# Performance work log

Measured on AMD Instinct MI355X. Metric: run time of the kernel, lower is better.

The kernel has to match this reference:

```python
import jax, jax.numpy as jnp
import numpy as np

U, I, T, D, A = 100000, 50000, 512, 64, 64
B, RU, RI = 2048, 50, 50


def _xavier(key, shape):
    fan_in, fan_out = shape[0], shape[1]
    lim = jnp.sqrt(6.0 / (fan_in + fan_out)).astype(jnp.float32)
    return jax.random.uniform(key, shape, jnp.float32, -lim, lim)


def setup_inputs() -> dict:
    key = jax.random.key(0)
    ks = jax.random.split(key, 16)
    return {
        "user": jax.random.randint(ks[0], (B,), 0, U),
        "item": jax.random.randint(ks[1], (B,), 0, I),
        "user_r_topic": jax.random.uniform(ks[2], (B, RU, T), jnp.float32),
        "item_r_topic": jax.random.uniform(ks[3], (B, RI, T), jnp.float32),
        "user_embed_w": 0.05 * jax.random.normal(ks[4], (U, D), jnp.float32),
        "item_embed_w": 0.05 * jax.random.normal(ks[5], (I, D), jnp.float32),
        "user_att_w": 0.05 * jax.random.normal(ks[6], (U, D), jnp.float32),
        "item_att_w": 0.05 * jax.random.normal(ks[7], (I, D), jnp.float32),
        "topic_embed_w": 0.05 * jax.random.normal(ks[8], (T, D), jnp.float32),
        "fc_u_w": _xavier(ks[9], (D, A)), "fc_u_b": jnp.zeros((A,), jnp.float32),
        "fc_ru_w": _xavier(ks[10], (D, A)), "fc_ru_b": jnp.zeros((A,), jnp.float32),
        "fc_i_w": _xavier(ks[11], (D, A)), "fc_i_b": jnp.zeros((A,), jnp.float32),
        "fc_ri_w": _xavier(ks[12], (D, A)), "fc_ri_b": jnp.zeros((A,), jnp.float32),
        "h_u_w": _xavier(ks[13], (A, 1)), "h_u_b": jnp.zeros((1,), jnp.float32),
        "h_i_w": _xavier(ks[14], (A, 1)), "h_i_b": jnp.zeros((1,), jnp.float32),
        "fc_pre_w": _xavier(ks[15], (2 * D, 1)), "fc_pre_b": jnp.zeros((1,), jnp.float32),
    }


def _branch(ids, emb_w, att_w, r_topic, topic_w, fc_a_w, fc_a_b, fc_r_w, fc_r_b, h_w, h_b):
    # embedding lookups
    emb = emb_w[ids]            # [B, D]
    att = att_w[ids]            # [B, D]
    # broadcast mul + sum over topics == matmul with topic table: [B, R, D]
    review = jnp.einsum("brt,td->brd", r_topic, topic_w)
    # attention scores over reviews
    s = jax.nn.relu((att @ fc_a_w + fc_a_b)[:, None, :] + review @ fc_r_w + fc_r_b)
    w = jax.nn.softmax((s @ h_w)[..., 0] + h_b[0], axis=1)   # [B, R]
    feat = jnp.einsum("br,brd->bd", w, review)               # attention pooling
    # (feat[:,None,:] * topic_emphasize).sum(dim=1) == feat * topic_w.sum(0)
    feat = feat * jnp.sum(topic_w, axis=0)
    return emb, feat


def reference(user, item, user_r_topic, item_r_topic,
              user_embed_w, item_embed_w, user_att_w, item_att_w, topic_embed_w,
              fc_u_w, fc_u_b, fc_ru_w, fc_ru_b, fc_i_w, fc_i_b, fc_ri_w, fc_ri_b,
              h_u_w, h_u_b, h_i_w, h_i_b, fc_pre_w, fc_pre_b):
    u_emb, u_feat = _branch(user, user_embed_w, user_att_w, user_r_topic, topic_embed_w,
                            fc_u_w, fc_u_b, fc_ru_w, fc_ru_b, h_u_w, h_u_b)
    i_emb, i_feat = _branch(item, item_embed_w, item_att_w, item_r_topic, topic_embed_w,
                            fc_i_w, fc_i_b, fc_ri_w, fc_ri_b, h_i_w, h_i_b)
    tmp = jnp.concatenate([u_feat + u_emb, i_feat + i_emb], axis=1)  # [B, 2D]
    pred = jax.nn.relu(tmp @ fc_pre_w + fc_pre_b)                    # [B, 1]
    return pred[:, 0]
```

## Files before the change

kernel.cpp:

```cpp
#include <hip/hip_runtime.h>
#include <cstdint>
#include <cstddef>

#define NB 2048
#define NT 512
#define ND 64
#define NR 50
#define NE 2
#define REVP 68
#define BH 32768

typedef __attribute__((ext_vector_type(8))) short bf16x8;
typedef __attribute__((ext_vector_type(4))) float f32x4;

__device__ inline unsigned short f2bf_rne(float x) {
    unsigned int u = __float_as_uint(x);
    u += 0x7fffu + ((u >> 16) & 1u);
    return (unsigned short)(u >> 16);
}

__device__ inline bf16x8 cvt8_rne(float4 v0, float4 v1) {
    union { unsigned int u[4]; bf16x8 v; } P;
    asm("v_cvt_pk_bf16_f32 %0, %1, %2" : "=v"(P.u[0]) : "v"(v0.x), "v"(v0.y));
    asm("v_cvt_pk_bf16_f32 %0, %1, %2" : "=v"(P.u[1]) : "v"(v0.z), "v"(v0.w));
    asm("v_cvt_pk_bf16_f32 %0, %1, %2" : "=v"(P.u[2]) : "v"(v1.x), "v"(v1.y));
    asm("v_cvt_pk_bf16_f32 %0, %1, %2" : "=v"(P.u[3]) : "v"(v1.z), "v"(v1.w));
    return P.v;
}

__device__ inline void gload16(const void* gsrc, void* ldst) {
    __builtin_amdgcn_global_load_lds(
        (const __attribute__((address_space(1))) unsigned int*)gsrc,
        (__attribute__((address_space(3))) unsigned int*)ldst, 16, 0, 0);
}

__global__ __launch_bounds__(256) void prep_kernel(
    const float* __restrict__ tw,
    const float* __restrict__ fc_u_w, const float* __restrict__ fc_ru_w,
    const float* __restrict__ fc_i_w, const float* __restrict__ fc_ri_w,
    unsigned short* __restrict__ bhi,
    unsigned short* __restrict__ fuhi, unsigned short* __restrict__ fihi)
{
    int i = blockIdx.x * 256 + threadIdx.x;
    if (i < 32768) {
        int j  = i & 7;
        int l  = (i >> 3) & 63;
        int n  = (i >> 9) & 3;
        int kk = i >> 11;
        int t = kk * 32 + ((l >> 4) << 3) + j;
        int d = n * 16 + (l & 15);
        bhi[i] = f2bf_rne(tw[t * ND + d]);
    } else {
        int q = i - 32768;
        int br = q >> 13;
        int e = q & 8191;
        int j  = e & 7;
        int l  = (e >> 3) & 63;
        int n  = (e >> 9) & 3;
        int kk = e >> 11;
        int k = kk * 32 + ((l >> 4) << 3) + j;
        int col = n * 16 + (l & 15);
        const float* W = (k < 64) ? (br ? fc_ri_w : fc_ru_w)
                                  : (br ? fc_i_w  : fc_u_w);
        unsigned short hi = f2bf_rne(W[(k & 63) * ND + col]);
        if (br) fihi[e] = hi; else fuhi[e] = hi;
    }
}

__global__ __launch_bounds__(256) void colsum_kernel(const float* __restrict__ tw,
                                                     float* __restrict__ colsum) {
    __shared__ float part[4][ND];
    int d = threadIdx.x & 63, p = threadIdx.x >> 6;
    float s = 0.f;
    for (int t = p; t < NT; t += 4) s += tw[t * ND + d];
    part[p][d] = s;
    __syncthreads();
    if (threadIdx.x < ND)
        colsum[d] = part[0][d] + part[1][d] + part[2][d] + part[3][d];
}

#define AISS2(T, e, COL)                                                       \
    float4 aA_##T##_0, aA_##T##_1;                                             \
    {                                                                          \
        const float* _p = arowp[e] + (size_t)rowc * NT + (COL);                \
        asm volatile("global_load_dwordx4 %0, %1, off"                         \
                     : "=v"(aA_##T##_0) : "v"(_p) : "memory");                 \
        asm volatile("global_load_dwordx4 %0, %1, off"                         \
                     : "=v"(aA_##T##_1) : "v"(_p + 4) : "memory");             \
    }
#define AISS8(T, e, h, qh)                                                     \
    AISS2(T##_0, e, (h) * 256 + ((qh) * 4 + 0) * 32 + g * 8)                   \
    AISS2(T##_1, e, (h) * 256 + ((qh) * 4 + 1) * 32 + g * 8)                   \
    AISS2(T##_2, e, (h) * 256 + ((qh) * 4 + 2) * 32 + g * 8)                   \
    AISS2(T##_3, e, (h) * 256 + ((qh) * 4 + 3) * 32 + g * 8)

#define ARET(T, N)                                                             \
    union { unsigned int u[4]; bf16x8 v; } fr_##T;                             \
    asm volatile("s_waitcnt vmcnt(" #N ")\n\t"                                 \
                 "v_cvt_pk_bf16_f32 %0, %4, %5\n\t"                            \
                 "v_cvt_pk_bf16_f32 %1, %6, %7\n\t"                            \
                 "v_cvt_pk_bf16_f32 %2, %8, %9\n\t"                            \
                 "v_cvt_pk_bf16_f32 %3, %10, %11"                              \
                 : "=&v"(fr_##T.u[0]), "=&v"(fr_##T.u[1]),                     \
                   "=&v"(fr_##T.u[2]), "=&v"(fr_##T.u[3])                      \
                 : "v"(aA_##T##_0.x), "v"(aA_##T##_0.y),                       \
                   "v"(aA_##T##_0.z), "v"(aA_##T##_0.w),                       \
                   "v"(aA_##T##_1.x), "v"(aA_##T##_1.y),                       \
                   "v"(aA_##T##_1.z), "v"(aA_##T##_1.w)                        \
                 : "memory");
#define ARETQ(T0, T1)                                                          \
    ARET(T0##_0, 14) ARET(T0##_1, 12) ARET(T0##_2, 10) ARET(T0##_3, 8)         \
    ARET(T1##_0, 6)  ARET(T1##_1, 4)  ARET(T1##_2, 2)  ARET(T1##_3, 0)
#define QCOMP(T0, T1, qh)                                                      \
    kstep((qh) * 4 + 0, fr_##T0##_0.v, fr_##T1##_0.v);                         \
    kstep((qh) * 4 + 1, fr_##T0##_1.v, fr_##T1##_1.v);                         \
    kstep((qh) * 4 + 2, fr_##T0##_2.v, fr_##T1##_2.v);                         \
    kstep((qh) * 4 + 3, fr_##T0##_3.v, fr_##T1##_3.v);

__global__ __launch_bounds__(256, 3) void branch_kernel(
    const int* __restrict__ user, const int* __restrict__ item,
    const float* __restrict__ user_r_topic, const float* __restrict__ item_r_topic,
    const float* __restrict__ user_embed_w, const float* __restrict__ item_embed_w,
    const float* __restrict__ user_att_w, const float* __restrict__ item_att_w,
    const unsigned short* __restrict__ bhi,
    const unsigned short* __restrict__ fuhi, const unsigned short* __restrict__ fihi,
    const float* __restrict__ fc_u_b, const float* __restrict__ fc_ru_b,
    const float* __restrict__ fc_i_b, const float* __restrict__ fc_ri_b,
    const float* __restrict__ h_u_w, const float* __restrict__ h_u_b,
    const float* __restrict__ h_i_w, const float* __restrict__ h_i_b,
    const float* __restrict__ colsum,
    float* __restrict__ u_vec, float* __restrict__ i_vec)
{
    __shared__ __align__(16) unsigned char arena[BH];
    __shared__ float lds_logit[NE][NR + 2];

    const int tid = threadIdx.x, wave = tid >> 6, lane = tid & 63;
    const int g = lane >> 4, c16 = lane & 15;

    const int E0 = blockIdx.x * NE;
    const int branch = E0 >> 11;

    const int*   ids     = branch ? item           : user;
    const float* r_topic = branch ? item_r_topic   : user_r_topic;
    const float* emb_w   = branch ? item_embed_w   : user_embed_w;
    const float* att_w   = branch ? item_att_w     : user_att_w;
    const unsigned short* fhi = branch ? fihi : fuhi;
    const float* fc_a_b  = branch ? fc_i_b         : fc_u_b;
    const float* fc_r_b  = branch ? fc_ri_b        : fc_ru_b;
    const float* h_w     = branch ? h_i_w          : h_u_w;
    const float* h_b     = branch ? h_i_b          : h_u_b;
    float*       out_vec = branch ? i_vec          : u_vec;

    const int rowg = wave * 16 + c16;
    const int rowc = rowg < NR ? rowg : NR - 1;

    int bidx[NE], idv[NE];
    const float* arowp[NE];
#pragma unroll
    for (int e = 0; e < NE; ++e) {
        bidx[e] = (E0 + e) & (NB - 1);
        idv[e]  = ids[bidx[e]];
        arowp[e] = r_topic + (size_t)bidx[e] * NR * NT;
    }

    auto stageB = [&](int h) {
        const unsigned char* src = (const unsigned char*)bhi + (size_t)h * BH;
#pragma unroll
        for (int i = 0; i < 8; ++i) {
            size_t off = (size_t)(i * 256 + tid) * 16;
            gload16(src + off, arena + off);
        }
    };

    f32x4 acc[NE][4];
#pragma unroll
    for (int e = 0; e < NE; ++e)
#pragma unroll
        for (int n = 0; n < 4; ++n) acc[e][n] = (f32x4){0.f, 0.f, 0.f, 0.f};

    auto kstep = [&](int klq, bf16x8 f0, bf16x8 f1) {
#pragma unroll
        for (int n = 0; n < 4; ++n) {
            bf16x8 bh = *reinterpret_cast<const bf16x8*>(
                arena + (size_t)((klq * 4 + n) * 64 + lane) * 16);
            acc[0][n] = __builtin_amdgcn_mfma_f32_16x16x32_bf16(f0, bh, acc[0][n], 0, 0, 0);
            acc[1][n] = __builtin_amdgcn_mfma_f32_16x16x32_bf16(f1, bh, acc[1][n], 0, 0, 0);
        }
    };

    stageB(0);
    AISS8(h0q0e0, 0, 0, 0) AISS8(h0q0e1, 1, 0, 0)
    asm volatile("s_waitcnt vmcnt(16)" ::: "memory");
    __builtin_amdgcn_sched_barrier(0);
    __builtin_amdgcn_s_barrier();
    __builtin_amdgcn_sched_barrier(0);
    ARETQ(h0q0e0, h0q0e1)
    QCOMP(h0q0e0, h0q0e1, 0)
    AISS8(h0q1e0, 0, 0, 1) AISS8(h0q1e1, 1, 0, 1)
    ARETQ(h0q1e0, h0q1e1)
    QCOMP(h0q1e0, h0q1e1, 1)
    __builtin_amdgcn_sched_barrier(0);
    __builtin_amdgcn_s_barrier();
    __builtin_amdgcn_sched_barrier(0);

    stageB(1);
    AISS8(h1q0e0, 0, 1, 0) AISS8(h1q0e1, 1, 1, 0)
    asm volatile("s_waitcnt vmcnt(16)" ::: "memory");
    __builtin_amdgcn_sched_barrier(0);
    __builtin_amdgcn_s_barrier();
    __builtin_amdgcn_sched_barrier(0);
    ARETQ(h1q0e0, h1q0e1)
    QCOMP(h1q0e0, h1q0e1, 0)
    AISS8(h1q1e0, 0, 1, 1) AISS8(h1q1e1, 1, 1, 1)
    ARETQ(h1q1e0, h1q1e1)
    QCOMP(h1q1e0, h1q1e1, 1)

    __syncthreads();
    float (*rev)[NR][REVP] = reinterpret_cast<float(*)[NR][REVP]>(arena);
#pragma unroll
    for (int e = 0; e < NE; ++e)
#pragma unroll
        for (int n = 0; n < 4; ++n)
#pragma unroll
            for (int r4 = 0; r4 < 4; ++r4) {
                int r = wave * 16 + g * 4 + r4;
                if (r < NR) rev[e][r][n * 16 + c16] = acc[e][n][r4];
            }

    f32x4 s4[NE][4];
#pragma unroll
    for (int e = 0; e < NE; ++e)
#pragma unroll
        for (int n = 0; n < 4; ++n) s4[e][n] = (f32x4){0.f, 0.f, 0.f, 0.f};

#pragma unroll
    for (int kk2 = 0; kk2 < 4; ++kk2) {
        bf16x8 bh[4];
#pragma unroll
        for (int n = 0; n < 4; ++n)
            bh[n] = *(reinterpret_cast<const bf16x8*>(fhi + (size_t)(kk2 * 4 + n) * 512) + lane);
#pragma unroll
        for (int e = 0; e < NE; ++e) {
            bf16x8 ah;
            if (kk2 < 2) {
                const float* rp = &rev[e][rowc][kk2 * 32 + g * 8];
                ah = cvt8_rne(*reinterpret_cast<const float4*>(rp),
                              *reinterpret_cast<const float4*>(rp + 4));
            } else {
                const float* ap = att_w + (size_t)idv[e] * ND + (kk2 - 2) * 32 + g * 8;
                ah = cvt8_rne(*reinterpret_cast<const float4*>(ap),
                              *reinterpret_cast<const float4*>(ap + 4));
            }
#pragma unroll
            for (int n = 0; n < 4; ++n)
                s4[e][n] = __builtin_amdgcn_mfma_f32_16x16x32_bf16(ah, bh[n], s4[e][n], 0, 0, 0);
        }
    }

    const float hb = h_b[0];
#pragma unroll
    for (int e = 0; e < NE; ++e) {
        float p0 = 0.f, p1 = 0.f, p2 = 0.f, p3 = 0.f;
#pragma unroll
        for (int n = 0; n < 4; ++n) {
            float hwn = h_w[n * 16 + c16];
            float bs = fc_r_b[n * 16 + c16] + fc_a_b[n * 16 + c16];
            p0 = fmaf(fmaxf(s4[e][n][0] + bs, 0.f), hwn, p0);
            p1 = fmaf(fmaxf(s4[e][n][1] + bs, 0.f), hwn, p1);
            p2 = fmaf(fmaxf(s4[e][n][2] + bs, 0.f), hwn, p2);
            p3 = fmaf(fmaxf(s4[e][n][3] + bs, 0.f), hwn, p3);
        }
#pragma unroll
        for (int off = 1; off < 16; off <<= 1) {
            p0 += __shfl_xor(p0, off);
            p1 += __shfl_xor(p1, off);
            p2 += __shfl_xor(p2, off);
            p3 += __shfl_xor(p3, off);
        }
        if (c16 == 0) {
            int rb = wave * 16 + g * 4;
            if (rb + 0 < NR) lds_logit[e][rb + 0] = p0 + hb;
            if (rb + 1 < NR) lds_logit[e][rb + 1] = p1 + hb;
            if (rb + 2 < NR) lds_logit[e][rb + 2] = p2 + hb;
            if (rb + 3 < NR) lds_logit[e][rb + 3] = p3 + hb;
        }
    }
    __syncthreads();

    if (wave < NE) {
        const int e = wave;
        const int b = bidx[e];
        const int id = idv[e];
        float m = -1e30f;
        for (int r = 0; r < NR; ++r) m = fmaxf(m, lds_logit[e][r]);
        float sum = 0.f;
        for (int r = 0; r < NR; ++r) sum += __expf(lds_logit[e][r] - m);
        float inv = 1.f / sum;
        float feat = 0.f;
        for (int r = 0; r < NR; ++r)
            feat = fmaf(__expf(lds_logit[e][r] - m), rev[e][r][lane], feat);
        feat *= inv;
        out_vec[(size_t)b * ND + lane] = feat * colsum[lane] + emb_w[(size_t)id * ND + lane];
    }
}

__global__ __launch_bounds__(64) void final_kernel(
    const float* __restrict__ u_vec, const float* __restrict__ i_vec,
    const float* __restrict__ fc_pre_w, const float* __restrict__ fc_pre_b,
    float* __restrict__ out)
{
    int b = blockIdx.x, lane = threadIdx.x;
    float v = u_vec[(size_t)b * ND + lane] * fc_pre_w[lane]
            + i_vec[(size_t)b * ND + lane] * fc_pre_w[ND + lane];
#pragma unroll
    for (int off = 32; off; off >>= 1) v += __shfl_xor(v, off);
    if (lane == 0) out[b] = fmaxf(v + fc_pre_b[0], 0.f);
}

extern "C" void kernel_launch(void* const* d_in, const int* in_sizes, int n_in,
                              void* d_out, int out_size, void* d_ws, size_t ws_size,
                              hipStream_t stream) {
    (void)in_sizes; (void)n_in; (void)out_size; (void)ws_size;

    const int*   user         = (const int*)d_in[0];
    const int*   item         = (const int*)d_in[1];
    const float* user_r_topic = (const float*)d_in[2];
    const float* item_r_topic = (const float*)d_in[3];
    const float* user_embed_w = (const float*)d_in[4];
    const float* item_embed_w = (const float*)d_in[5];
    const float* user_att_w   = (const float*)d_in[6];
    const float* item_att_w   = (const float*)d_in[7];
    const float* topic_w      = (const float*)d_in[8];
    const float* fc_u_w       = (const float*)d_in[9];
    const float* fc_u_b       = (const float*)d_in[10];
    const float* fc_ru_w      = (const float*)d_in[11];
    const float* fc_ru_b      = (const float*)d_in[12];
    const float* fc_i_w       = (const float*)d_in[13];
    const float* fc_i_b       = (const float*)d_in[14];
    const float* fc_ri_w      = (const float*)d_in[15];
    const float* fc_ri_b      = (const float*)d_in[16];
    const float* h_u_w        = (const float*)d_in[17];
    const float* h_u_b        = (const float*)d_in[18];
    const float* h_i_w        = (const float*)d_in[19];
    const float* h_i_b        = (const float*)d_in[20];
    const float* fc_pre_w     = (const float*)d_in[21];
    const float* fc_pre_b     = (const float*)d_in[22];

    unsigned short* bhi  = (unsigned short*)d_ws;
    unsigned short* fuhi = bhi + 32768;
    unsigned short* fihi = fuhi + 8192;
    float* colsum = (float*)(fihi + 8192);
    float* u_vec  = colsum + 64;
    float* i_vec  = u_vec + NB * ND;

    prep_kernel<<<192, 256, 0, stream>>>(topic_w, fc_u_w, fc_ru_w, fc_i_w, fc_ri_w,
                                         bhi, fuhi, fihi);
    colsum_kernel<<<1, 256, 0, stream>>>(topic_w, colsum);

    branch_kernel<<<(2 * NB) / NE, 256, 0, stream>>>(
        user, item, user_r_topic, item_r_topic,
        user_embed_w, item_embed_w, user_att_w, item_att_w,
        bhi, fuhi, fihi,
        fc_u_b, fc_ru_b, fc_i_b, fc_ri_b,
        h_u_w, h_u_b, h_i_w, h_i_b,
        colsum, u_vec, i_vec);

    final_kernel<<<NB, 64, 0, stream>>>(u_vec, i_vec, fc_pre_w, fc_pre_b,
                                        (float*)d_out);
}
```

Before: 124.1 us.

## Process four entities per block with full B tile staged once in LDS

Each block now handles four batch entities instead of two and stages the entire 64KB bf16 topic-weight table into LDS in one pass, so the second half-stage and its barrier go away. A-operand loads are software-pipelined per entity: each entity's fragments are converted while the next entity's loads are in flight. This cuts the number of blocks and amortizes the B-table load over twice as many entities. In exchange, occupancy drops (launch bounds from 3 to 2 blocks per CU, larger LDS), and more loads are kept in flight, which raises register pressure.

New measurement: 127.8 us. 1.03x slower.

```diff
diff --git a/kernel.cpp b/kernel.cpp
--- a/kernel.cpp
+++ b/kernel.cpp
@@ -6,9 +6,9 @@
 #define NT 512
 #define ND 64
 #define NR 50
-#define NE 2
+#define NE 4
 #define REVP 68
-#define BH 32768
+#define BFULL 65536
 
 typedef __attribute__((ext_vector_type(8))) short bf16x8;
 typedef __attribute__((ext_vector_type(4))) float f32x4;
@@ -88,13 +88,17 @@
         asm volatile("global_load_dwordx4 %0, %1, off"                         \
                      : "=v"(aA_##T##_1) : "v"(_p + 4) : "memory");             \
     }
-#define AISS8(T, e, h, qh)                                                     \
-    AISS2(T##_0, e, (h) * 256 + ((qh) * 4 + 0) * 32 + g * 8)                   \
-    AISS2(T##_1, e, (h) * 256 + ((qh) * 4 + 1) * 32 + g * 8)                   \
-    AISS2(T##_2, e, (h) * 256 + ((qh) * 4 + 2) * 32 + g * 8)                   \
-    AISS2(T##_3, e, (h) * 256 + ((qh) * 4 + 3) * 32 + g * 8)
-
-#define ARET(T, N)                                                             \
+#define AISS16(T, e, h)                                                        \
+    AISS2(T##_0, e, (h) * 256 + 0 * 32 + g * 8)                                \
+    AISS2(T##_1, e, (h) * 256 + 1 * 32 + g * 8)                                \
+    AISS2(T##_2, e, (h) * 256 + 2 * 32 + g * 8)                                \
+    AISS2(T##_3, e, (h) * 256 + 3 * 32 + g * 8)                                \
+    AISS2(T##_4, e, (h) * 256 + 4 * 32 + g * 8)                                \
+    AISS2(T##_5, e, (h) * 256 + 5 * 32 + g * 8)                                \
+    AISS2(T##_6, e, (h) * 256 + 6 * 32 + g * 8)                                \
+    AISS2(T##_7, e, (h) * 256 + 7 * 32 + g * 8)
+
+#define FRAG(T, N)                                                             \
     union { unsigned int u[4]; bf16x8 v; } fr_##T;                             \
     asm volatile("s_waitcnt vmcnt(" #N ")\n\t"                                 \
                  "v_cvt_pk_bf16_f32 %0, %4, %5\n\t"                            \
@@ -108,16 +112,19 @@
                    "v"(aA_##T##_1.x), "v"(aA_##T##_1.y),                       \
                    "v"(aA_##T##_1.z), "v"(aA_##T##_1.w)                        \
                  : "memory");
-#define ARETQ(T0, T1)                                                          \
-    ARET(T0##_0, 14) ARET(T0##_1, 12) ARET(T0##_2, 10) ARET(T0##_3, 8)         \
-    ARET(T1##_0, 6)  ARET(T1##_1, 4)  ARET(T1##_2, 2)  ARET(T1##_3, 0)
-#define QCOMP(T0, T1, qh)                                                      \
-    kstep((qh) * 4 + 0, fr_##T0##_0.v, fr_##T1##_0.v);                         \
-    kstep((qh) * 4 + 1, fr_##T0##_1.v, fr_##T1##_1.v);                         \
-    kstep((qh) * 4 + 2, fr_##T0##_2.v, fr_##T1##_2.v);                         \
-    kstep((qh) * 4 + 3, fr_##T0##_3.v, fr_##T1##_3.v);
-
-__global__ __launch_bounds__(256, 3) void branch_kernel(
+#define ARETH(T)                                                               \
+    FRAG(T##_0, 30) FRAG(T##_1, 28) FRAG(T##_2, 26) FRAG(T##_3, 24)            \
+    FRAG(T##_4, 22) FRAG(T##_5, 20) FRAG(T##_6, 18) FRAG(T##_7, 16)
+#define ARETL(T)                                                               \
+    FRAG(T##_0, 14) FRAG(T##_1, 12) FRAG(T##_2, 10) FRAG(T##_3, 8)             \
+    FRAG(T##_4, 6)  FRAG(T##_5, 4)  FRAG(T##_6, 2)  FRAG(T##_7, 0)
+#define QCOMP8(T, e, h)                                                        \
+    kstep((h) * 8 + 0, fr_##T##_0.v, e); kstep((h) * 8 + 1, fr_##T##_1.v, e);  \
+    kstep((h) * 8 + 2, fr_##T##_2.v, e); kstep((h) * 8 + 3, fr_##T##_3.v, e);  \
+    kstep((h) * 8 + 4, fr_##T##_4.v, e); kstep((h) * 8 + 5, fr_##T##_5.v, e);  \
+    kstep((h) * 8 + 6, fr_##T##_6.v, e); kstep((h) * 8 + 7, fr_##T##_7.v, e);
+
+__global__ __launch_bounds__(256, 2) void branch_kernel(
     const int* __restrict__ user, const int* __restrict__ item,
     const float* __restrict__ user_r_topic, const float* __restrict__ item_r_topic,
     const float* __restrict__ user_embed_w, const float* __restrict__ item_embed_w,
@@ -131,7 +138,7 @@
     const float* __restrict__ colsum,
     float* __restrict__ u_vec, float* __restrict__ i_vec)
 {
-    __shared__ __align__(16) unsigned char arena[BH];
+    __shared__ __align__(16) unsigned char arena[BFULL];
     __shared__ float lds_logit[NE][NR + 2];
 
     const int tid = threadIdx.x, wave = tid >> 6, lane = tid & 63;
@@ -163,57 +170,43 @@
         arowp[e] = r_topic + (size_t)bidx[e] * NR * NT;
     }
 
-    auto stageB = [&](int h) {
-        const unsigned char* src = (const unsigned char*)bhi + (size_t)h * BH;
-#pragma unroll
-        for (int i = 0; i < 8; ++i) {
-            size_t off = (size_t)(i * 256 + tid) * 16;
-            gload16(src + off, arena + off);
-        }
-    };
-
     f32x4 acc[NE][4];
 #pragma unroll
     for (int e = 0; e < NE; ++e)
 #pragma unroll
         for (int n = 0; n < 4; ++n) acc[e][n] = (f32x4){0.f, 0.f, 0.f, 0.f};
 
-    auto kstep = [&](int klq, bf16x8 f0, bf16x8 f1) {
+    auto kstep = [&](int kk, bf16x8 f, int e) {
 #pragma unroll
         for (int n = 0; n < 4; ++n) {
             bf16x8 bh = *reinterpret_cast<const bf16x8*>(
-                arena + (size_t)((klq * 4 + n) * 64 + lane) * 16);
-            acc[0][n] = __builtin_amdgcn_mfma_f32_16x16x32_bf16(f0, bh, acc[0][n], 0, 0, 0);
-            acc[1][n] = __builtin_amdgcn_mfma_f32_16x16x32_bf16(f1, bh, acc[1][n], 0, 0, 0);
+                arena + (size_t)((kk * 4 + n) * 64 + lane) * 16);
+            acc[e][n] = __builtin_amdgcn_mfma_f32_16x16x32_bf16(f, bh, acc[e][n], 0, 0, 0);
         }
     };
 
-    stageB(0);
-    AISS8(h0q0e0, 0, 0, 0) AISS8(h0q0e1, 1, 0, 0)
-    asm volatile("s_waitcnt vmcnt(16)" ::: "memory");
+    {
+#pragma unroll
+        for (int i = 0; i < 16; ++i) {
+            size_t off = (size_t)(i * 256 + tid) * 16;
+            gload16((const unsigned char*)bhi + off, arena + off);
+        }
+    }
+    AISS16(A0, 0, 0)
+    AISS16(A1, 1, 0)
+    asm volatile("s_waitcnt vmcnt(32)" ::: "memory");
     __builtin_amdgcn_sched_barrier(0);
     __builtin_amdgcn_s_barrier();
     __builtin_amdgcn_sched_barrier(0);
-    ARETQ(h0q0e0, h0q0e1)
-    QCOMP(h0q0e0, h0q0e1, 0)
-    AISS8(h0q1e0, 0, 0, 1) AISS8(h0q1e1, 1, 0, 1)
-    ARETQ(h0q1e0, h0q1e1)
-    QCOMP(h0q1e0, h0q1e1, 1)
-    __builtin_amdgcn_sched_barrier(0);
-    __builtin_amdgcn_s_barrier();
-    __builtin_amdgcn_sched_barrier(0);
-
-    stageB(1);
-    AISS8(h1q0e0, 0, 1, 0) AISS8(h1q0e1, 1, 1, 0)
-    asm volatile("s_waitcnt vmcnt(16)" ::: "memory");
-    __builtin_amdgcn_sched_barrier(0);
-    __builtin_amdgcn_s_barrier();
-    __builtin_amdgcn_sched_barrier(0);
-    ARETQ(h1q0e0, h1q0e1)
-    QCOMP(h1q0e0, h1q0e1, 0)
-    AISS8(h1q1e0, 0, 1, 1) AISS8(h1q1e1, 1, 1, 1)
-    ARETQ(h1q1e0, h1q1e1)
-    QCOMP(h1q1e0, h1q1e1, 1)
+
+    ARETH(A0) AISS16(A2, 2, 0) QCOMP8(A0, 0, 0)
+    ARETH(A1) AISS16(A3, 3, 0) QCOMP8(A1, 1, 0)
+    ARETH(A2) AISS16(B0, 0, 1) QCOMP8(A2, 2, 0)
+    ARETH(A3) AISS16(B1, 1, 1) QCOMP8(A3, 3, 0)
+    ARETH(B0) AISS16(B2, 2, 1) QCOMP8(B0, 0, 1)
+    ARETH(B1) AISS16(B3, 3, 1) QCOMP8(B1, 1, 1)
+    ARETH(B2)                  QCOMP8(B2, 2, 1)
+    ARETL(B3)                  QCOMP8(B3, 3, 1)
 
     __syncthreads();
     float (*rev)[NR][REVP] = reinterpret_cast<float(*)[NR][REVP]>(arena);
@@ -287,7 +280,7 @@
     }
     __syncthreads();
 
-    if (wave < NE) {
+    {
         const int e = wave;
         const int b = bidx[e];
         const int id = idv[e];
```

## Software-pipeline A-fragment loads one chunk ahead of MFMA compute

Applied to the files above, without the earlier changes.

Restructures the streaming of the review-topic rows so each 8-load chunk for one branch is issued before the previous chunk is converted and fed to the MFMAs. Compute is split per branch, and the vmcnt waits are retuned to match. This keeps more global loads in flight while matrix instructions run, hiding memory latency behind compute. In exchange it keeps more live registers for outstanding loads, which could pressure occupancy at 3 waves per SIMD. It also relies on hand-counted vmcnt values being correct.

Result: no change. 125.0 us (+0.7%).

```diff
diff --git a/kernel.cpp b/kernel.cpp
--- a/kernel.cpp
+++ b/kernel.cpp
@@ -94,7 +94,7 @@
     AISS2(T##_2, e, (h) * 256 + ((qh) * 4 + 2) * 32 + g * 8)                   \
     AISS2(T##_3, e, (h) * 256 + ((qh) * 4 + 3) * 32 + g * 8)
 
-#define ARET(T, N)                                                             \
+#define FRAG(T, N)                                                             \
     union { unsigned int u[4]; bf16x8 v; } fr_##T;                             \
     asm volatile("s_waitcnt vmcnt(" #N ")\n\t"                                 \
                  "v_cvt_pk_bf16_f32 %0, %4, %5\n\t"                            \
@@ -108,14 +108,13 @@
                    "v"(aA_##T##_1.x), "v"(aA_##T##_1.y),                       \
                    "v"(aA_##T##_1.z), "v"(aA_##T##_1.w)                        \
                  : "memory");
-#define ARETQ(T0, T1)                                                          \
-    ARET(T0##_0, 14) ARET(T0##_1, 12) ARET(T0##_2, 10) ARET(T0##_3, 8)         \
-    ARET(T1##_0, 6)  ARET(T1##_1, 4)  ARET(T1##_2, 2)  ARET(T1##_3, 0)
-#define QCOMP(T0, T1, qh)                                                      \
-    kstep((qh) * 4 + 0, fr_##T0##_0.v, fr_##T1##_0.v);                         \
-    kstep((qh) * 4 + 1, fr_##T0##_1.v, fr_##T1##_1.v);                         \
-    kstep((qh) * 4 + 2, fr_##T0##_2.v, fr_##T1##_2.v);                         \
-    kstep((qh) * 4 + 3, fr_##T0##_3.v, fr_##T1##_3.v);
+#define RETQ22(T) FRAG(T##_0, 22) FRAG(T##_1, 20) FRAG(T##_2, 18) FRAG(T##_3, 16)
+#define RETQ30(T) FRAG(T##_0, 30) FRAG(T##_1, 28) FRAG(T##_2, 26) FRAG(T##_3, 24)
+#define RETQ14(T) FRAG(T##_0, 14) FRAG(T##_1, 12) FRAG(T##_2, 10) FRAG(T##_3, 8)
+#define RETQ6(T)  FRAG(T##_0, 6)  FRAG(T##_1, 4)  FRAG(T##_2, 2)  FRAG(T##_3, 0)
+#define QCOMP4(T, e, qh)                                                       \
+    kstep((qh) * 4 + 0, fr_##T##_0.v, e); kstep((qh) * 4 + 1, fr_##T##_1.v, e);\
+    kstep((qh) * 4 + 2, fr_##T##_2.v, e); kstep((qh) * 4 + 3, fr_##T##_3.v, e);
 
 __global__ __launch_bounds__(256, 3) void branch_kernel(
     const int* __restrict__ user, const int* __restrict__ item,
@@ -178,42 +177,48 @@
 #pragma unroll
         for (int n = 0; n < 4; ++n) acc[e][n] = (f32x4){0.f, 0.f, 0.f, 0.f};
 
-    auto kstep = [&](int klq, bf16x8 f0, bf16x8 f1) {
+    auto kstep = [&](int klq, bf16x8 f, int e) {
 #pragma unroll
         for (int n = 0; n < 4; ++n) {
             bf16x8 bh = *reinterpret_cast<const bf16x8*>(
                 arena + (size_t)((klq * 4 + n) * 64 + lane) * 16);
-            acc[0][n] = __builtin_amdgcn_mfma_f32_16x16x32_bf16(f0, bh, acc[0][n], 0, 0, 0);
-            acc[1][n] = __builtin_amdgcn_mfma_f32_16x16x32_bf16(f1, bh, acc[1][n], 0, 0, 0);
+            acc[e][n] = __builtin_amdgcn_mfma_f32_16x16x32_bf16(f, bh, acc[e][n], 0, 0, 0);
         }
     };
 
     stageB(0);
-    AISS8(h0q0e0, 0, 0, 0) AISS8(h0q0e1, 1, 0, 0)
+    AISS8(c0, 0, 0, 0) AISS8(c1, 1, 0, 0)
     asm volatile("s_waitcnt vmcnt(16)" ::: "memory");
     __builtin_amdgcn_sched_barrier(0);
     __builtin_amdgcn_s_barrier();
     __builtin_amdgcn_sched_barrier(0);
-    ARETQ(h0q0e0, h0q0e1)
-    QCOMP(h0q0e0, h0q0e1, 0)
-    AISS8(h0q1e0, 0, 0, 1) AISS8(h0q1e1, 1, 0, 1)
-    ARETQ(h0q1e0, h0q1e1)
-    QCOMP(h0q1e0, h0q1e1, 1)
+
+    AISS8(c2, 0, 0, 1)
+    RETQ22(c0) QCOMP4(c0, 0, 0)
+    AISS8(c3, 1, 0, 1)
+    RETQ22(c1) QCOMP4(c1, 1, 0)
+    AISS8(c4, 0, 1, 0)
+    RETQ22(c2) QCOMP4(c2, 0, 1)
+    AISS8(c5, 1, 1, 0)
+    RETQ22(c3) QCOMP4(c3, 1, 1)
     __builtin_amdgcn_sched_barrier(0);
     __builtin_amdgcn_s_barrier();
     __builtin_amdgcn_sched_barrier(0);
 
     stageB(1);
-    AISS8(h1q0e0, 0, 1, 0) AISS8(h1q0e1, 1, 1, 0)
-    asm volatile("s_waitcnt vmcnt(16)" ::: "memory");
+    AISS8(c6, 0, 1, 1)
+    RETQ30(c4)
+    RETQ22(c5)
+    asm volatile("s_waitcnt vmcnt(8)" ::: "memory");
     __builtin_amdgcn_sched_barrier(0);
     __builtin_amdgcn_s_barrier();
     __builtin_amdgcn_sched_barrier(0);
-    ARETQ(h1q0e0, h1q0e1)
-    QCOMP(h1q0e0, h1q0e1, 0)
-    AISS8(h1q1e0, 0, 1, 1) AISS8(h1q1e1, 1, 1, 1)
-    ARETQ(h1q1e0, h1q1e1)
-    QCOMP(h1q1e0, h1q1e1, 1)
+
+    QCOMP4(c4, 0, 0)
+    AISS8(c7, 1, 1, 1)
+    QCOMP4(c5, 1, 0)
+    RETQ14(c6) QCOMP4(c6, 0, 1)
+    RETQ6(c7)  QCOMP4(c7, 1, 1)
 
     __syncthreads();
     float (*rev)[NR][REVP] = reinterpret_cast<float(*)[NR][REVP]>(arena);
```
